# Optimization experiments

Measured on AMD Instinct MI355X. Metric: run time of the kernel, lower is better.

## Reference

```python
import jax, jax.numpy as jnp
import numpy as np

NUM_BATCH = 8  # GroupNormalization(num_batch=num_groups) with num_groups=8
EPS = 1e-6


def setup_inputs() -> dict:
    key = jax.random.key(0)
    k1, k2, k3 = jax.random.split(key, 3)
    b, h, w, c = 32, 32, 32, 256
    x = jax.random.normal(k1, (b, h, w, c), dtype=jnp.float32)
    gamma = jnp.ones((c,), dtype=jnp.float32)
    beta = jnp.zeros((c,), dtype=jnp.float32)
    w_qkv = jax.random.normal(k2, (c, 3 * c), dtype=jnp.float32) * 0.02
    w_out = jax.random.normal(k3, (c, c), dtype=jnp.float32) * 0.02
    return {"x": x, "gamma": gamma, "beta": beta, "w_qkv": w_qkv, "w_out": w_out}


def reference(x, gamma, beta, w_qkv, w_out):
    b, h, w, c = x.shape
    # --- GroupNormalization (exact quirky semantics of the source) ---
    # num_groups = c // num_batch; reshape to [-1, num_groups, group_size]
    # -> per-(b,h,w)-pixel normalization over contiguous channel groups.
    ng = c // NUM_BATCH          # 32 groups
    gs = c // ng                 # 8 channels per group
    g = x.reshape(-1, ng, gs)
    mu = jnp.mean(g, axis=-1, keepdims=True)
    var = jnp.mean(jnp.square(g - mu), axis=-1, keepdims=True)
    xn = ((g - mu) / jnp.sqrt(var + EPS)).reshape(x.shape)
    xn = gamma * xn + beta
    # --- 1x1 conv to qkv (bias-free) ---
    qkv = jnp.einsum('bhwc,cd->bhwd', xn, w_qkv)  # [b,h,w,3c]
    q, k, v = jnp.split(qkv, 3, axis=-1)
    # self_attention=True branch: tie q=k=v to their mean
    t = (v + q + k) / 3.0
    q = k = v = t
    # --- exact reshapes from the source (raw reshapes, not transposes) ---
    q = jnp.transpose(q, (0, 3, 1, 2)).reshape(b, h * w, c)  # [b,hw,c]
    k = k.reshape(b, c, h * w)                               # [b,c,hw]
    v = jnp.transpose(v, (0, 3, 1, 2)).reshape(b, h * w, c)  # [b,hw,c]
    scores = jnp.matmul(q, k) * (c ** -0.5)                  # [b,hw,hw]
    attn = jax.nn.softmax(scores, axis=-1)
    # NOTE: source passes transpose_a=float (truthy) -> attention is transposed
    out = jnp.matmul(jnp.swapaxes(attn, 1, 2), v)            # [b,hw,c]
    out = out.reshape(b, h, w, c)
    return jnp.einsum('bhwc,cd->bhwd', out, w_out) + x
```

## Files before the change

### kernel.cpp

```cpp
#include <hip/hip_runtime.h>

typedef unsigned short u16;
typedef unsigned char u8;
typedef long long i64;
typedef __bf16 bf16x8 __attribute__((ext_vector_type(8)));
typedef float f32x4 __attribute__((ext_vector_type(4)));
typedef u16 u16x8 __attribute__((ext_vector_type(8)));

#define GLD16(g, l) __builtin_amdgcn_global_load_lds( \
    (const __attribute__((address_space(1))) void*)(g), \
    (__attribute__((address_space(3))) void*)(l), 16, 0, 0)
#define VMW(N) asm volatile("s_waitcnt vmcnt(" #N ")" ::: "memory")

__device__ __forceinline__ float bf2f(u16 u) {
  return __uint_as_float(((unsigned)u) << 16);
}
__device__ __forceinline__ u16 f2bf(float f) {
  unsigned u = __float_as_uint(f);
  return (u16)((u + 0x7fffu + ((u >> 16) & 1u)) >> 16);
}
__device__ __forceinline__ u8 f8e_sw(float v) {
  unsigned u = __float_as_uint(v);
  unsigned s = (u >> 24) & 0x80u;
  u &= 0x7fffffffu;
  if (u < 0x3c000000u) return (u8)s;
  int b = (int)((u + 0x7FFFFu + ((u >> 20) & 1u)) >> 20) - 960;
  b = b < 8 ? 8 : (b > 126 ? 126 : b);
  return (u8)(b | s);
}
__device__ __forceinline__ float f8d_sw(u8 b) {
  if (!(b & 0x7f)) return 0.0f;
  float v = __uint_as_float((((unsigned)(b & 0x7fu)) << 20) + 0x3C000000u);
  return (b & 0x80u) ? -v : v;
}
__device__ __forceinline__ unsigned pk4(float a, float b, float c, float d) {
#if __has_builtin(__builtin_amdgcn_cvt_pk_fp8_f32)
  int r = __builtin_amdgcn_cvt_pk_fp8_f32(a, b, 0, false);
  r = __builtin_amdgcn_cvt_pk_fp8_f32(c, d, r, true);
  return (unsigned)r;
#else
  return (unsigned)f8e_sw(a) | ((unsigned)f8e_sw(b) << 8) |
         ((unsigned)f8e_sw(c) << 16) | ((unsigned)f8e_sw(d) << 24);
#endif
}
__device__ __forceinline__ float f8df(u8 b) {
#if __has_builtin(__builtin_amdgcn_cvt_f32_fp8)
  return __builtin_amdgcn_cvt_f32_fp8((int)b, 0);
#else
  return f8d_sw(b);
#endif
}
__device__ __forceinline__ int sig(int r) { return (r ^ (r >> 3)) & 7; }

__global__ void combine_w(const float* __restrict__ wqkv, const float* __restrict__ wout,
                          u16* __restrict__ wtT, u16* __restrict__ woutT) {
  int c = blockIdx.x, d = threadIdx.x;
  float t = (wqkv[c * 768 + d] + wqkv[c * 768 + 256 + d] + wqkv[c * 768 + 512 + d]) * (1.0f / 3.0f);
  wtT[d * 256 + c] = f2bf(t);
  woutT[d * 256 + c] = f2bf(wout[c * 256 + d]);
}

__global__ __launch_bounds__(512) void gnT(
    const float* __restrict__ x, const float* __restrict__ gamma,
    const float* __restrict__ beta, const u16* __restrict__ wtT,
    u8* __restrict__ Q8, u8* __restrict__ Kt8) {
  __shared__ u16 lA[2][64 * 64];
  __shared__ u16 lB[2][256 * 64];
  const int m0 = blockIdx.x * 64;
  const int z = m0 >> 10;
  const int t = threadIdx.x, lane = t & 63;
  const int w = t >> 6, wr = w >> 2, wc = w & 3;
  f32x4 acc[2][4] = {};

#define GNT_STAGE(B, K0)                                                        \
  {                                                                             \
    _Pragma("unroll") for (int ch = 0; ch < 4; ch++) {                          \
      int flat = ch * 512 + t, row = flat >> 3, slot = flat & 7;                \
      GLD16(wtT + (size_t)row * 256 + (K0) + (slot ^ sig(row)) * 8,             \
            lB[B] + flat * 8);                                                  \
    }                                                                           \
    int row = t >> 3, grp = t & 7;                                              \
    const float* xp = x + (size_t)(m0 + row) * 256 + (K0) + grp * 8;            \
    float4 a = *(const float4*)xp, b = *(const float4*)(xp + 4);                \
    float mu = (a.x + a.y + a.z + a.w + b.x + b.y + b.z + b.w) * 0.125f;        \
    float d0 = a.x - mu, d1 = a.y - mu, d2 = a.z - mu, d3 = a.w - mu;           \
    float d4 = b.x - mu, d5 = b.y - mu, d6 = b.z - mu, d7 = b.w - mu;           \
    float var = (d0 * d0 + d1 * d1 + d2 * d2 + d3 * d3 +                        \
                 d4 * d4 + d5 * d5 + d6 * d6 + d7 * d7) * 0.125f;               \
    float rs = rsqrtf(var + 1e-6f);                                             \
    const float4 g0 = *(const float4*)(gamma + (K0) + grp * 8);                 \
    const float4 g1 = *(const float4*)(gamma + (K0) + grp * 8 + 4);             \
    const float4 e0 = *(const float4*)(beta + (K0) + grp * 8);                  \
    const float4 e1 = *(const float4*)(beta + (K0) + grp * 8 + 4);              \
    u16x8 o;                                                                    \
    o[0] = f2bf(g0.x * (d0 * rs) + e0.x); o[1] = f2bf(g0.y * (d1 * rs) + e0.y); \
    o[2] = f2bf(g0.z * (d2 * rs) + e0.z); o[3] = f2bf(g0.w * (d3 * rs) + e0.w); \
    o[4] = f2bf(g1.x * (d4 * rs) + e1.x); o[5] = f2bf(g1.y * (d5 * rs) + e1.y); \
    o[6] = f2bf(g1.z * (d6 * rs) + e1.z); o[7] = f2bf(g1.w * (d7 * rs) + e1.w); \
    *(u16x8*)(lA[B] + row * 64 + (grp ^ sig(row)) * 8) = o;                     \
  }

  GNT_STAGE(0, 0);
  __syncthreads();
  for (int it = 0; it < 4; it++) {
    if (it < 3) { GNT_STAGE((it + 1) & 1, (it + 1) * 64); }
    const u16* la = lA[it & 1];
    const u16* lb = lB[it & 1];
#pragma unroll
    for (int kk = 0; kk < 2; kk++) {
      bf16x8 af[2], bfr[4];
#pragma unroll
      for (int mi = 0; mi < 2; mi++) {
        int m = wr * 32 + mi * 16 + (lane & 15);
        af[mi] = *(const bf16x8*)(la + m * 64 + ((kk * 32 + (lane >> 4) * 8) ^ (sig(m) << 3)));
      }
#pragma unroll
      for (int ni = 0; ni < 4; ni++) {
        int n = wc * 64 + ni * 16 + (lane & 15);
        bfr[ni] = *(const bf16x8*)(lb + n * 64 + ((kk * 32 + (lane >> 4) * 8) ^ (sig(n) << 3)));
      }
#pragma unroll
      for (int mi = 0; mi < 2; mi++)
#pragma unroll
        for (int ni = 0; ni < 4; ni++)
          acc[mi][ni] = __builtin_amdgcn_mfma_f32_16x16x32_bf16(af[mi], bfr[ni], acc[mi][ni], 0, 0, 0);
    }
    __syncthreads();
  }

  const int rb = m0 + wr * 32 + ((lane >> 4) << 2);
  const int cb = wc * 64 + (lane & 15);
  u8* kt = (u8*)lB[0];
  u8* qtile = (u8*)lB[1];
#pragma unroll
  for (int mi = 0; mi < 2; mi++)
#pragma unroll
    for (int ni = 0; ni < 4; ni++) {
      int P0 = rb + mi * 16, c = cb + ni * 16;
      int pl = P0 - m0;
      unsigned pk = pk4(acc[mi][ni][0], acc[mi][ni][1], acc[mi][ni][2], acc[mi][ni][3]);
#pragma unroll
      for (int j = 0; j < 4; j++)
        kt[(j * 256 + c) * 16 + (pl >> 2)] = (u8)(pk >> (8 * j));
      *(unsigned*)(qtile + c * 80 + pl) = pk;
    }
  __syncthreads();
  const int ckb = (m0 & 1023) >> 2;
  u8* Kz = Kt8 + (size_t)z * 262144;
  u8* Qz = Q8 + (size_t)z * 262144;
#pragma unroll
  for (int r2 = 0; r2 < 2; r2++) {
    int r = t * 2 + r2;
    uint4 v = *(const uint4*)(kt + r * 16);
    *(uint4*)(Kz + (size_t)r * 256 + ckb) = v;
  }
#pragma unroll
  for (int ph = 0; ph < 2; ph++) {
    int idx = ph * 512 + t, c = idx >> 2, q = idx & 3;
    uint4 v = *(const uint4*)(qtile + c * 80 + q * 16);
    *(uint4*)(Qz + (size_t)c * 1024 + (m0 & 1023) + q * 16) = v;
  }
#undef GNT_STAGE
}

__global__ __launch_bounds__(256) void gemm_s8(
    const u8* __restrict__ Q8, const u8* __restrict__ Kt8,
    u8* __restrict__ Et, float* __restrict__ partials) {
  __shared__ u8 lA[128 * 256];
  __shared__ u8 lB[128 * 256];
  const int z = blockIdx.x;
  const int mb = blockIdx.y & 7, pb = blockIdx.y >> 3;
  const u8* Az = Q8 + (size_t)z * 262144;
  const u8* Bz = Kt8 + (size_t)z * 262144;
  u8* Ez = Et + (size_t)z * 1048576;
  const int m0 = mb * 128, n0 = pb * 128;
  const int t = threadIdx.x, lane = t & 63;
  const int wr = (t >> 6) >> 1, wc = (t >> 6) & 1;
  f32x4 acc[4][4] = {};

#pragma unroll
  for (int ch = 0; ch < 8; ch++) {
    int flat = ch * 256 + t, row = flat >> 4, slot = flat & 15;
    GLD16(Az + (size_t)(m0 + row) * 256 + (slot ^ sig(row)) * 16, lA + flat * 16);
  }
#pragma unroll
  for (int ch = 0; ch < 8; ch++) {
    int flat = ch * 256 + t, row = flat >> 4, slot = flat & 15;
    GLD16(Bz + (size_t)(n0 + row) * 256 + (slot ^ sig(row)) * 16, lB + flat * 16);
  }
  __syncthreads();
#pragma unroll
  for (int kk = 0; kk < 8; kk++) {
    i64 af[4], bfv[4];
    int koff = kk * 32 + (lane >> 4) * 8;
#pragma unroll
    for (int mi = 0; mi < 4; mi++) {
      int m = wr * 64 + mi * 16 + (lane & 15);
      af[mi] = *(const i64*)(lA + m * 256 + (koff ^ (sig(m) << 4)));
    }
#pragma unroll
    for (int ni = 0; ni < 4; ni++) {
      int n = wc * 64 + ni * 16 + (lane & 15);
      bfv[ni] = *(const i64*)(lB + n * 256 + (koff ^ (sig(n) << 4)));
    }
#pragma unroll
    for (int mi = 0; mi < 4; mi++)
#pragma unroll
      for (int ni = 0; ni < 4; ni++)
        acc[mi][ni] = __builtin_amdgcn_mfma_f32_16x16x32_fp8_fp8(af[mi], bfv[ni], acc[mi][ni], 0, 0, 0);
  }
  __syncthreads();
  u8* ldsC = lA;
  const int rbl = wr * 64 + ((lane >> 4) << 2);
  const int cbl = wc * 64 + (lane & 15);
  const float SCL = 0.0625f * 1.44269504089f;
  float ps[4][4] = {};
#pragma unroll
  for (int mi = 0; mi < 4; mi++)
#pragma unroll
    for (int ni = 0; ni < 4; ni++) {
      int pl = cbl + ni * 16, ib = rbl + mi * 16;
      float e0 = exp2f(acc[mi][ni][0] * SCL);
      float e1 = exp2f(acc[mi][ni][1] * SCL);
      float e2 = exp2f(acc[mi][ni][2] * SCL);
      float e3 = exp2f(acc[mi][ni][3] * SCL);
      ps[mi][0] += e0; ps[mi][1] += e1; ps[mi][2] += e2; ps[mi][3] += e3;
      *(unsigned*)(ldsC + pl * 128 + (ib ^ ((pl & 7) << 4))) = pk4(e0, e1, e2, e3);
    }
#pragma unroll
  for (int mi = 0; mi < 4; mi++)
#pragma unroll
    for (int j = 0; j < 4; j++) {
      float v = ps[mi][j];
      v += __shfl_xor(v, 1); v += __shfl_xor(v, 2);
      v += __shfl_xor(v, 4); v += __shfl_xor(v, 8);
      if ((lane & 15) == 0)
        partials[(size_t)(z * 1024 + m0 + rbl + mi * 16 + j) * 16 + pb * 2 + wc] = v;
    }
  __syncthreads();
#pragma unroll
  for (int ph = 0; ph < 4; ph++) {
    int pl = ph * 32 + (t >> 3), ich = (t & 7) * 16;
    uint4 v = *(const uint4*)(ldsC + pl * 128 + (ich ^ ((pl & 7) << 4)));
    *(uint4*)(Ez + (size_t)(n0 + pl) * 1024 + m0 + ich) = v;
  }
}

__global__ __launch_bounds__(256) void qt8(
    const u8* __restrict__ Q8, const float* __restrict__ partials, u8* __restrict__ Qt) {
  __shared__ u8 tile[64][260];
  __shared__ float rv[64];
  const int z = blockIdx.y, i0 = blockIdx.x * 64;
  const u8* src = Q8 + (size_t)z * 262144;
  u8* dst = Qt + (size_t)z * 262144;
  const int t = threadIdx.x;
#pragma unroll
  for (int q = 0; q < 4; q++) {
    uint4 v = *(const uint4*)(src + (size_t)(i0 + (t >> 2)) * 256 + (t & 3) * 64 + q * 16);
    *(uint4*)(&tile[t >> 2][(t & 3) * 64 + q * 16]) = v;
  }
  if (t < 64) {
    const float4* p = (const float4*)(partials + (size_t)(z * 1024 + i0 + t) * 16);
    float4 a = p[0], b = p[1], c = p[2], d = p[3];
    float s = ((a.x + a.y) + (a.z + a.w)) + ((b.x + b.y) + (b.z + b.w)) +
              ((c.x + c.y) + (c.z + c.w)) + ((d.x + d.y) + (d.z + d.w));
    rv[t] = 1024.0f / s;
  }
  __syncthreads();
#pragma unroll
  for (int q = 0; q < 4; q++) {
    unsigned wd[4];
#pragma unroll
    for (int d = 0; d < 4; d++) {
      float f[4];
#pragma unroll
      for (int e = 0; e < 4; e++) {
        int i = q * 16 + d * 4 + e;
        f[e] = f8df(tile[i][t]) * rv[i];
      }
      wd[d] = pk4(f[0], f[1], f[2], f[3]);
    }
    uint4 v = {wd[0], wd[1], wd[2], wd[3]};
    *(uint4*)(dst + (size_t)t * 1024 + i0 + q * 16) = v;
  }
}

__global__ __launch_bounds__(512) void gemm_of(
    const u8* __restrict__ Et, const u8* __restrict__ Qt,
    const u16* __restrict__ woutT, const float* __restrict__ x,
    float* __restrict__ C) {
  __shared__ char smem[131072];
  const int z = blockIdx.x;
  const int m0 = blockIdx.y * 128;
  const u8* Az = Et + (size_t)z * 1048576;
  const u8* Bz = Qt + (size_t)z * 262144;
  const int t = threadIdx.x, lane = t & 63;
  const int w = t >> 6, wr = w >> 2, wc = w & 3;
  f32x4 acc[4][4] = {};

#define O8_STAGE(B, K0)                                                       \
  {                                                                           \
    u8* la_ = (u8*)smem + (B) * 16384;                                        \
    u8* lb_ = (u8*)smem + 32768 + (B) * 32768;                                \
    _Pragma("unroll") for (int ch = 0; ch < 2; ch++) {                        \
      int flat = ch * 512 + t, row = flat >> 3, slot = flat & 7;              \
      GLD16(Az + (size_t)(m0 + row) * 1024 + (K0) + (slot ^ sig(row)) * 16,   \
            la_ + flat * 16);                                                 \
    }                                                                         \
    _Pragma("unroll") for (int ch = 0; ch < 4; ch++) {                        \
      int flat = ch * 512 + t, row = flat >> 3, slot = flat & 7;              \
      GLD16(Bz + (size_t)row * 1024 + (K0) + (slot ^ sig(row)) * 16,          \
            lb_ + flat * 16);                                                 \
    }                                                                         \
  }

  O8_STAGE(0, 0);
  for (int it = 0; it < 8; it++) {
    if (it < 7) {
      O8_STAGE((it + 1) & 1, (it + 1) * 128);
      VMW(6);
    } else {
      VMW(0);
    }
    __builtin_amdgcn_sched_barrier(0);
    __builtin_amdgcn_s_barrier();
    __builtin_amdgcn_sched_barrier(0);
    const u8* la = (const u8*)smem + (it & 1) * 16384;
    const u8* lb = (const u8*)smem + 32768 + (it & 1) * 32768;
#pragma unroll
    for (int kk = 0; kk < 4; kk++) {
      i64 af[4], bfv[4];
      int koff = kk * 32 + (lane >> 4) * 8;
#pragma unroll
      for (int mi = 0; mi < 4; mi++) {
        int m = wr * 64 + mi * 16 + (lane & 15);
        af[mi] = *(const i64*)(la + m * 128 + (koff ^ (sig(m) << 4)));
      }
#pragma unroll
      for (int ni = 0; ni < 4; ni++) {
        int n = wc * 64 + ni * 16 + (lane & 15);
        bfv[ni] = *(const i64*)(lb + n * 128 + (koff ^ (sig(n) << 4)));
      }
#pragma unroll
      for (int mi = 0; mi < 4; mi++)
#pragma unroll
        for (int ni = 0; ni < 4; ni++)
          acc[mi][ni] = __builtin_amdgcn_mfma_f32_16x16x32_fp8_fp8(af[mi], bfv[ni], acc[mi][ni], 0, 0, 0);
    }
    __builtin_amdgcn_s_barrier();
  }
#undef O8_STAGE

#define W_STAGE(B, K0)                                                        \
  {                                                                           \
    u16* wb_ = (u16*)(smem + 65536 + (B) * 32768);                            \
    _Pragma("unroll") for (int ch = 0; ch < 4; ch++) {                        \
      int flat = ch * 512 + t, row = flat >> 3, slot = flat & 7;              \
      GLD16(woutT + (size_t)row * 256 + (K0) + (slot ^ sig(row)) * 8,         \
            (u8*)wb_ + flat * 16);                                            \
    }                                                                         \
  }
  W_STAGE(0, 0);
  {
    const int rbl = wr * 64 + ((lane >> 4) << 2);
    const int cbl = wc * 64 + (lane & 15);
#pragma unroll
    for (int mi = 0; mi < 4; mi++)
#pragma unroll
      for (int ni = 0; ni < 4; ni++)
#pragma unroll
        for (int j = 0; j < 4; j++) {
          int pl = rbl + mi * 16 + j, c = cbl + ni * 16;
          int byteoff = (pl * 512 + c * 2) ^ ((pl & 7) << 4);
          *(u16*)(smem + byteoff) = f2bf(acc[mi][ni][j] * (1.0f / 1024.0f));
        }
  }
  asm volatile("s_waitcnt lgkmcnt(0)" ::: "memory");
  __builtin_amdgcn_sched_barrier(0);
  __builtin_amdgcn_s_barrier();
  __builtin_amdgcn_sched_barrier(0);

  f32x4 acc2[4][4] = {};
  for (int it2 = 0; it2 < 4; it2++) {
    if (it2 < 3) {
      W_STAGE((it2 + 1) & 1, (it2 + 1) * 64);
      VMW(4);
    } else {
      VMW(0);
    }
    __builtin_amdgcn_sched_barrier(0);
    __builtin_amdgcn_s_barrier();
    __builtin_amdgcn_sched_barrier(0);
    const u16* lb = (const u16*)(smem + 65536 + (it2 & 1) * 32768);
#pragma unroll
    for (int kk = 0; kk < 2; kk++) {
      bf16x8 af[4], bfr[4];
#pragma unroll
      for (int mi = 0; mi < 4; mi++) {
        int m = wr * 64 + mi * 16 + (lane & 15);
        int kg = it2 * 64 + kk * 32 + (lane >> 4) * 8;
        af[mi] = *(const bf16x8*)(smem + ((m * 512 + kg * 2) ^ ((m & 7) << 4)));
      }
#pragma unroll
      for (int ni = 0; ni < 4; ni++) {
        int n = wc * 64 + ni * 16 + (lane & 15);
        bfr[ni] = *(const bf16x8*)(lb + n * 64 + ((kk * 32 + (lane >> 4) * 8) ^ (sig(n) << 3)));
      }
#pragma unroll
      for (int mi = 0; mi < 4; mi++)
#pragma unroll
        for (int ni = 0; ni < 4; ni++)
          acc2[mi][ni] = __builtin_amdgcn_mfma_f32_16x16x32_bf16(af[mi], bfr[ni], acc2[mi][ni], 0, 0, 0);
    }
    __builtin_amdgcn_s_barrier();
  }
#undef W_STAGE

  {
    const int rbl = wr * 64 + ((lane >> 4) << 2);
    const int cbl = wc * 64 + (lane & 15);
#pragma unroll
    for (int mi = 0; mi < 4; mi++)
#pragma unroll
      for (int ni = 0; ni < 4; ni++)
#pragma unroll
        for (int j = 0; j < 4; j++) {
          int pl = rbl + mi * 16 + j, c = cbl + ni * 16;
          *(float*)(smem + ((pl * 1024 + c * 4) ^ ((pl & 7) << 4))) = acc2[mi][ni][j];
        }
    __syncthreads();
    const size_t base = (size_t)(z * 1024 + m0) * 256;
#pragma unroll
    for (int pi = 0; pi < 16; pi++) {
      int flat = pi * 512 + t;
      int row = flat >> 6, ch = flat & 63;
      f32x4 a = *(const f32x4*)(smem + row * 1024 + ((ch * 16) ^ ((row & 7) << 4)));
      const float4 xv = *(const float4*)(x + base + (size_t)flat * 4);
      float4 o;
      o.x = a[0] + xv.x; o.y = a[1] + xv.y; o.z = a[2] + xv.z; o.w = a[3] + xv.w;
      *(float4*)(C + base + (size_t)flat * 4) = o;
    }
  }
}

extern "C" void kernel_launch(void* const* d_in, const int* in_sizes, int n_in,
                              void* d_out, int out_size, void* d_ws, size_t ws_size,
                              hipStream_t stream) {
  (void)in_sizes; (void)n_in; (void)out_size; (void)ws_size;
  const float* x = (const float*)d_in[0];
  const float* gamma = (const float*)d_in[1];
  const float* beta = (const float*)d_in[2];
  const float* wqkv = (const float*)d_in[3];
  const float* wout = (const float*)d_in[4];
  float* outp = (float*)d_out;

  char* ws = (char*)d_ws;
  const size_t MB = 1024 * 1024;
  u16* wtT = (u16*)(ws + 0);
  u16* woutT = (u16*)(ws + (128 << 10));
  float* partials = (float*)(ws + (512 << 10));
  u8* Q8 = (u8*)(ws + 3 * MB);
  u8* Kt8 = (u8*)(ws + 12 * MB);
  u8* Qt = (u8*)(ws + 21 * MB);
  u8* Et = (u8*)(ws + 30 * MB);

  combine_w<<<256, 256, 0, stream>>>(wqkv, wout, wtT, woutT);
  gnT<<<512, 512, 0, stream>>>(x, gamma, beta, wtT, Q8, Kt8);
  gemm_s8<<<dim3(32, 64), 256, 0, stream>>>(Q8, Kt8, Et, partials);
  qt8<<<dim3(16, 32), 256, 0, stream>>>(Q8, partials, Qt);
  gemm_of<<<dim3(32, 8), 512, 0, stream>>>(Et, Qt, woutT, x, outp);
}
```

Baseline: 91.36 us.

## Split gemm_s8 K loads into two pipelined stages; halve gemm_of M tile

gemm_s8 now loads its K dimension in two 128-byte halves into double-buffered LDS, so the first half's MFMAs can start while the second half is still loading. gemm_of shrinks its M tile from 128 to 64 rows, doubling the grid to 512 blocks, cutting LDS use to 80KB and adding launch_bounds(512,4). Its output-projection stage moves to 8 narrower bf16 K steps with a new swizzle for the weight tile. Both kernels raise wave priority with s_setprio around MFMA sections. The smaller tile re-reads Qt and woutT more often per output row.

```diff
diff --git a/kernel.cpp b/kernel.cpp
--- a/kernel.cpp
+++ b/kernel.cpp
@@ -11,6 +11,8 @@
     (const __attribute__((address_space(1))) void*)(g), \
     (__attribute__((address_space(3))) void*)(l), 16, 0, 0)
 #define VMW(N) asm volatile("s_waitcnt vmcnt(" #N ")" ::: "memory")
+#define SCHB __builtin_amdgcn_sched_barrier(0)
+#define SBAR __builtin_amdgcn_s_barrier()
 
 __device__ __forceinline__ float bf2f(u16 u) {
   return __uint_as_float(((unsigned)u) << 16);
@@ -51,6 +53,7 @@
 #endif
 }
 __device__ __forceinline__ int sig(int r) { return (r ^ (r >> 3)) & 7; }
+__device__ __forceinline__ int wkey(int r) { return (r ^ (r >> 2)) & 3; }
 
 __global__ void combine_w(const float* __restrict__ wqkv, const float* __restrict__ wout,
                           u16* __restrict__ wtT, u16* __restrict__ woutT) {
@@ -166,8 +169,8 @@
 __global__ __launch_bounds__(256) void gemm_s8(
     const u8* __restrict__ Q8, const u8* __restrict__ Kt8,
     u8* __restrict__ Et, float* __restrict__ partials) {
-  __shared__ u8 lA[128 * 256];
-  __shared__ u8 lB[128 * 256];
+  __shared__ u8 lA[2][128 * 128];
+  __shared__ u8 lB[2][128 * 128];
   const int z = blockIdx.x;
   const int mb = blockIdx.y & 7, pb = blockIdx.y >> 3;
   const u8* Az = Q8 + (size_t)z * 262144;
@@ -178,39 +181,52 @@
   const int wr = (t >> 6) >> 1, wc = (t >> 6) & 1;
   f32x4 acc[4][4] = {};
 
-#pragma unroll
-  for (int ch = 0; ch < 8; ch++) {
-    int flat = ch * 256 + t, row = flat >> 4, slot = flat & 15;
-    GLD16(Az + (size_t)(m0 + row) * 256 + (slot ^ sig(row)) * 16, lA + flat * 16);
-  }
-#pragma unroll
-  for (int ch = 0; ch < 8; ch++) {
-    int flat = ch * 256 + t, row = flat >> 4, slot = flat & 15;
-    GLD16(Bz + (size_t)(n0 + row) * 256 + (slot ^ sig(row)) * 16, lB + flat * 16);
-  }
+#define S8_STAGE(B, K0)                                                       \
+  {                                                                           \
+    _Pragma("unroll") for (int ch = 0; ch < 4; ch++) {                        \
+      int flat = ch * 256 + t, row = flat >> 3, slot = flat & 7;              \
+      GLD16(Az + (size_t)(m0 + row) * 256 + (K0) + (slot ^ sig(row)) * 16,    \
+            lA[B] + flat * 16);                                               \
+    }                                                                         \
+    _Pragma("unroll") for (int ch = 0; ch < 4; ch++) {                        \
+      int flat = ch * 256 + t, row = flat >> 3, slot = flat & 7;              \
+      GLD16(Bz + (size_t)(n0 + row) * 256 + (K0) + (slot ^ sig(row)) * 16,    \
+            lB[B] + flat * 16);                                               \
+    }                                                                         \
+  }
+#define S8_COMP(LA, LB)                                                       \
+  _Pragma("unroll") for (int kk = 0; kk < 4; kk++) {                          \
+    i64 af[4], bfv[4];                                                        \
+    int koff = kk * 32 + (lane >> 4) * 8;                                     \
+    _Pragma("unroll") for (int mi = 0; mi < 4; mi++) {                        \
+      int m = wr * 64 + mi * 16 + (lane & 15);                                \
+      af[mi] = *(const i64*)((LA) + m * 128 + (koff ^ (sig(m) << 4)));        \
+    }                                                                         \
+    _Pragma("unroll") for (int ni = 0; ni < 4; ni++) {                        \
+      int n = wc * 64 + ni * 16 + (lane & 15);                                \
+      bfv[ni] = *(const i64*)((LB) + n * 128 + (koff ^ (sig(n) << 4)));       \
+    }                                                                         \
+    _Pragma("unroll") for (int mi = 0; mi < 4; mi++)                          \
+      _Pragma("unroll") for (int ni = 0; ni < 4; ni++)                        \
+        acc[mi][ni] = __builtin_amdgcn_mfma_f32_16x16x32_fp8_fp8(             \
+            af[mi], bfv[ni], acc[mi][ni], 0, 0, 0);                           \
+  }
+
+  S8_STAGE(0, 0);
+  S8_STAGE(1, 128);
+  VMW(8); SCHB; SBAR; SCHB;
+  __builtin_amdgcn_s_setprio(1);
+  S8_COMP(lA[0], lB[0]);
+  __builtin_amdgcn_s_setprio(0);
+  VMW(0); SCHB; SBAR; SCHB;
+  __builtin_amdgcn_s_setprio(1);
+  S8_COMP(lA[1], lB[1]);
+  __builtin_amdgcn_s_setprio(0);
   __syncthreads();
-#pragma unroll
-  for (int kk = 0; kk < 8; kk++) {
-    i64 af[4], bfv[4];
-    int koff = kk * 32 + (lane >> 4) * 8;
-#pragma unroll
-    for (int mi = 0; mi < 4; mi++) {
-      int m = wr * 64 + mi * 16 + (lane & 15);
-      af[mi] = *(const i64*)(lA + m * 256 + (koff ^ (sig(m) << 4)));
-    }
-#pragma unroll
-    for (int ni = 0; ni < 4; ni++) {
-      int n = wc * 64 + ni * 16 + (lane & 15);
-      bfv[ni] = *(const i64*)(lB + n * 256 + (koff ^ (sig(n) << 4)));
-    }
-#pragma unroll
-    for (int mi = 0; mi < 4; mi++)
-#pragma unroll
-      for (int ni = 0; ni < 4; ni++)
-        acc[mi][ni] = __builtin_amdgcn_mfma_f32_16x16x32_fp8_fp8(af[mi], bfv[ni], acc[mi][ni], 0, 0, 0);
-  }
-  __syncthreads();
-  u8* ldsC = lA;
+#undef S8_STAGE
+#undef S8_COMP
+
+  u8* ldsC = lA[0];
   const int rbl = wr * 64 + ((lane >> 4) << 2);
   const int cbl = wc * 64 + (lane & 15);
   const float SCL = 0.0625f * 1.44269504089f;
@@ -285,27 +301,27 @@
   }
 }
 
-__global__ __launch_bounds__(512) void gemm_of(
+__global__ __launch_bounds__(512, 4) void gemm_of(
     const u8* __restrict__ Et, const u8* __restrict__ Qt,
     const u16* __restrict__ woutT, const float* __restrict__ x,
     float* __restrict__ C) {
-  __shared__ char smem[131072];
+  __shared__ char smem[81920];
   const int z = blockIdx.x;
-  const int m0 = blockIdx.y * 128;
+  const int m0 = blockIdx.y * 64;
   const u8* Az = Et + (size_t)z * 1048576;
   const u8* Bz = Qt + (size_t)z * 262144;
   const int t = threadIdx.x, lane = t & 63;
   const int w = t >> 6, wr = w >> 2, wc = w & 3;
-  f32x4 acc[4][4] = {};
+  f32x4 acc[2][4] = {};
 
 #define O8_STAGE(B, K0)                                                       \
   {                                                                           \
-    u8* la_ = (u8*)smem + (B) * 16384;                                        \
-    u8* lb_ = (u8*)smem + 32768 + (B) * 32768;                                \
-    _Pragma("unroll") for (int ch = 0; ch < 2; ch++) {                        \
-      int flat = ch * 512 + t, row = flat >> 3, slot = flat & 7;              \
+    u8* la_ = (u8*)smem + (B) * 8192;                                         \
+    u8* lb_ = (u8*)smem + 16384 + (B) * 32768;                                \
+    {                                                                         \
+      int row = t >> 3, slot = t & 7;                                         \
       GLD16(Az + (size_t)(m0 + row) * 1024 + (K0) + (slot ^ sig(row)) * 16,   \
-            la_ + flat * 16);                                                 \
+            la_ + t * 16);                                                    \
     }                                                                         \
     _Pragma("unroll") for (int ch = 0; ch < 4; ch++) {                        \
       int flat = ch * 512 + t, row = flat >> 3, slot = flat & 7;              \
@@ -318,22 +334,21 @@
   for (int it = 0; it < 8; it++) {
     if (it < 7) {
       O8_STAGE((it + 1) & 1, (it + 1) * 128);
-      VMW(6);
+      VMW(5);
     } else {
       VMW(0);
     }
-    __builtin_amdgcn_sched_barrier(0);
-    __builtin_amdgcn_s_barrier();
-    __builtin_amdgcn_sched_barrier(0);
-    const u8* la = (const u8*)smem + (it & 1) * 16384;
-    const u8* lb = (const u8*)smem + 32768 + (it & 1) * 32768;
+    SCHB; SBAR; SCHB;
+    const u8* la = (const u8*)smem + (it & 1) * 8192;
+    const u8* lb = (const u8*)smem + 16384 + (it & 1) * 32768;
+    __builtin_amdgcn_s_setprio(1);
 #pragma unroll
     for (int kk = 0; kk < 4; kk++) {
-      i64 af[4], bfv[4];
+      i64 af[2], bfv[4];
       int koff = kk * 32 + (lane >> 4) * 8;
 #pragma unroll
-      for (int mi = 0; mi < 4; mi++) {
-        int m = wr * 64 + mi * 16 + (lane & 15);
+      for (int mi = 0; mi < 2; mi++) {
+        int m = wr * 32 + mi * 16 + (lane & 15);
         af[mi] = *(const i64*)(la + m * 128 + (koff ^ (sig(m) << 4)));
       }
 #pragma unroll
@@ -342,103 +357,100 @@
         bfv[ni] = *(const i64*)(lb + n * 128 + (koff ^ (sig(n) << 4)));
       }
 #pragma unroll
-      for (int mi = 0; mi < 4; mi++)
+      for (int mi = 0; mi < 2; mi++)
 #pragma unroll
         for (int ni = 0; ni < 4; ni++)
           acc[mi][ni] = __builtin_amdgcn_mfma_f32_16x16x32_fp8_fp8(af[mi], bfv[ni], acc[mi][ni], 0, 0, 0);
     }
-    __builtin_amdgcn_s_barrier();
+    __builtin_amdgcn_s_setprio(0);
+    SBAR;
   }
 #undef O8_STAGE
 
 #define W_STAGE(B, K0)                                                        \
   {                                                                           \
-    u16* wb_ = (u16*)(smem + 65536 + (B) * 32768);                            \
-    _Pragma("unroll") for (int ch = 0; ch < 4; ch++) {                        \
-      int flat = ch * 512 + t, row = flat >> 3, slot = flat & 7;              \
-      GLD16(woutT + (size_t)row * 256 + (K0) + (slot ^ sig(row)) * 8,         \
-            (u8*)wb_ + flat * 16);                                            \
+    u8* wb_ = (u8*)smem + 32768 + (B) * 16384;                                \
+    _Pragma("unroll") for (int ch = 0; ch < 2; ch++) {                        \
+      int flat = ch * 512 + t, row = flat >> 2, slot = flat & 3;              \
+      GLD16(woutT + (size_t)row * 256 + (K0) + (slot ^ wkey(row)) * 8,        \
+            wb_ + flat * 16);                                                 \
     }                                                                         \
   }
   W_STAGE(0, 0);
   {
-    const int rbl = wr * 64 + ((lane >> 4) << 2);
-    const int cbl = wc * 64 + (lane & 15);
-#pragma unroll
-    for (int mi = 0; mi < 4; mi++)
+#pragma unroll
+    for (int mi = 0; mi < 2; mi++)
 #pragma unroll
       for (int ni = 0; ni < 4; ni++)
 #pragma unroll
         for (int j = 0; j < 4; j++) {
-          int pl = rbl + mi * 16 + j, c = cbl + ni * 16;
+          int pl = wr * 32 + mi * 16 + ((lane >> 4) << 2) + j;
+          int c = wc * 64 + ni * 16 + (lane & 15);
           int byteoff = (pl * 512 + c * 2) ^ ((pl & 7) << 4);
           *(u16*)(smem + byteoff) = f2bf(acc[mi][ni][j] * (1.0f / 1024.0f));
         }
   }
   asm volatile("s_waitcnt lgkmcnt(0)" ::: "memory");
-  __builtin_amdgcn_sched_barrier(0);
-  __builtin_amdgcn_s_barrier();
-  __builtin_amdgcn_sched_barrier(0);
-
-  f32x4 acc2[4][4] = {};
-  for (int it2 = 0; it2 < 4; it2++) {
-    if (it2 < 3) {
-      W_STAGE((it2 + 1) & 1, (it2 + 1) * 64);
-      VMW(4);
+  SCHB; SBAR; SCHB;
+
+  f32x4 acc2[2][4] = {};
+  for (int it2 = 0; it2 < 8; it2++) {
+    if (it2 < 7) {
+      W_STAGE((it2 + 1) & 1, (it2 + 1) * 32);
+      VMW(2);
     } else {
       VMW(0);
     }
-    __builtin_amdgcn_sched_barrier(0);
-    __builtin_amdgcn_s_barrier();
-    __builtin_amdgcn_sched_barrier(0);
-    const u16* lb = (const u16*)(smem + 65536 + (it2 & 1) * 32768);
-#pragma unroll
-    for (int kk = 0; kk < 2; kk++) {
-      bf16x8 af[4], bfr[4];
-#pragma unroll
-      for (int mi = 0; mi < 4; mi++) {
-        int m = wr * 64 + mi * 16 + (lane & 15);
-        int kg = it2 * 64 + kk * 32 + (lane >> 4) * 8;
-        af[mi] = *(const bf16x8*)(smem + ((m * 512 + kg * 2) ^ ((m & 7) << 4)));
+    SCHB; SBAR; SCHB;
+    const u8* wb = (const u8*)smem + 32768 + (it2 & 1) * 16384;
+    __builtin_amdgcn_s_setprio(1);
+    {
+      bf16x8 af2[2], bfr[4];
+#pragma unroll
+      for (int mi = 0; mi < 2; mi++) {
+        int m = wr * 32 + mi * 16 + (lane & 15);
+        int kg = (it2 * 32 + (lane >> 4) * 8) * 2;
+        af2[mi] = *(const bf16x8*)(smem + ((m * 512 + kg) ^ ((m & 7) << 4)));
       }
 #pragma unroll
       for (int ni = 0; ni < 4; ni++) {
         int n = wc * 64 + ni * 16 + (lane & 15);
-        bfr[ni] = *(const bf16x8*)(lb + n * 64 + ((kk * 32 + (lane >> 4) * 8) ^ (sig(n) << 3)));
-      }
-#pragma unroll
-      for (int mi = 0; mi < 4; mi++)
+        int s = lane >> 4;
+        bfr[ni] = *(const bf16x8*)(wb + n * 64 + (s ^ wkey(n)) * 16);
+      }
+#pragma unroll
+      for (int mi = 0; mi < 2; mi++)
 #pragma unroll
         for (int ni = 0; ni < 4; ni++)
-          acc2[mi][ni] = __builtin_amdgcn_mfma_f32_16x16x32_bf16(af[mi], bfr[ni], acc2[mi][ni], 0, 0, 0);
-    }
-    __builtin_amdgcn_s_barrier();
+          acc2[mi][ni] = __builtin_amdgcn_mfma_f32_16x16x32_bf16(af2[mi], bfr[ni], acc2[mi][ni], 0, 0, 0);
+    }
+    __builtin_amdgcn_s_setprio(0);
+    SBAR;
   }
 #undef W_STAGE
 
   {
-    const int rbl = wr * 64 + ((lane >> 4) << 2);
-    const int cbl = wc * 64 + (lane & 15);
-#pragma unroll
-    for (int mi = 0; mi < 4; mi++)
+#pragma unroll
+    for (int mi = 0; mi < 2; mi++)
 #pragma unroll
       for (int ni = 0; ni < 4; ni++)
 #pragma unroll
         for (int j = 0; j < 4; j++) {
-          int pl = rbl + mi * 16 + j, c = cbl + ni * 16;
+          int pl = wr * 32 + mi * 16 + ((lane >> 4) << 2) + j;
+          int c = wc * 64 + ni * 16 + (lane & 15);
           *(float*)(smem + ((pl * 1024 + c * 4) ^ ((pl & 7) << 4))) = acc2[mi][ni][j];
         }
     __syncthreads();
-    const size_t base = (size_t)(z * 1024 + m0) * 256;
-#pragma unroll
-    for (int pi = 0; pi < 16; pi++) {
-      int flat = pi * 512 + t;
-      int row = flat >> 6, ch = flat & 63;
+    const size_t base = ((size_t)z * 1024 + m0) * 256;
+#pragma unroll
+    for (int pi = 0; pi < 8; pi++) {
+      int f4 = pi * 512 + t;
+      int row = f4 >> 6, ch = f4 & 63;
       f32x4 a = *(const f32x4*)(smem + row * 1024 + ((ch * 16) ^ ((row & 7) << 4)));
-      const float4 xv = *(const float4*)(x + base + (size_t)flat * 4);
+      const float4 xv = *(const float4*)(x + base + (size_t)f4 * 4);
       float4 o;
       o.x = a[0] + xv.x; o.y = a[1] + xv.y; o.z = a[2] + xv.z; o.w = a[3] + xv.w;
-      *(float4*)(C + base + (size_t)flat * 4) = o;
+      *(float4*)(C + base + (size_t)f4 * 4) = o;
     }
   }
 }
@@ -468,5 +480,5 @@
   gnT<<<512, 512, 0, stream>>>(x, gamma, beta, wtT, Q8, Kt8);
   gemm_s8<<<dim3(32, 64), 256, 0, stream>>>(Q8, Kt8, Et, partials);
   qt8<<<dim3(16, 32), 256, 0, stream>>>(Q8, partials, Qt);
-  gemm_of<<<dim3(32, 8), 512, 0, stream>>>(Et, Qt, woutT, x, outp);
-}
+  gemm_of<<<dim3(32, 16), 512, 0, stream>>>(Et, Qt, woutT, x, outp);
+}
```

After: 90.13 us. About the same (-1.3%).
